# Optimization experiments

Measured on AMD Instinct MI355X. Metric: run time of the kernel, lower is better.

## Reference

```python
import jax, jax.numpy as jnp
import numpy as np

N_USERS = 100000
N_ITEMS = 200000
N_NODES = N_USERS + N_ITEMS
EMB_DIM = 64
N_EDGES = 4000000
N_LAYERS = 2
BATCH = 8192
EMB_REG = 2.5e-5


def setup_inputs() -> dict:
    key = jax.random.key(0)
    k = jax.random.split(key, 7)
    return {
        "user_emb": jax.random.normal(k[0], (N_USERS, EMB_DIM), jnp.float32) * 0.1,
        "item_emb": jax.random.normal(k[1], (N_ITEMS, EMB_DIM), jnp.float32) * 0.1,
        "all_h": jax.random.randint(k[2], (N_EDGES,), 0, N_NODES, jnp.int64 if jax.config.jax_enable_x64 else jnp.int32),
        "all_t": jax.random.randint(k[3], (N_EDGES,), 0, N_NODES, jnp.int64 if jax.config.jax_enable_x64 else jnp.int32),
        "users": jax.random.randint(k[4], (BATCH,), 0, N_USERS),
        "pos_items": jax.random.randint(k[5], (BATCH,), 0, N_ITEMS),
        "neg_items": jax.random.randint(k[6], (BATCH,), 0, N_ITEMS),
    }


def _spmm(h, t, vals, x):
    # out[h] += vals * x[t]  over all edges; [N_NODES, D]
    return jax.ops.segment_sum(vals[:, None] * x[t], h, num_segments=N_NODES)


def reference(user_emb, item_emb, all_h, all_t, users, pos_items, neg_items):
    # symmetric normalization G = D^{-1/2} A D^{-1/2} on the edge list
    deg = jax.ops.segment_sum(jnp.ones((all_h.shape[0],), user_emb.dtype), all_h,
                              num_segments=N_NODES)
    dinv = jnp.where(deg > 0, deg ** -0.5, 0.0)
    g_vals = dinv[all_h] * dinv[all_t]

    # inference1: n_layers of SpMM with residual; sum over all layer outputs
    # (dropout p=0 on the main branch in the source -> identity)
    emb = jnp.concatenate([user_emb, item_emb], axis=0)  # [N, D]
    acc = emb
    for _ in range(N_LAYERS):
        emb = _spmm(all_h, all_t, g_vals, emb) + emb
        acc = acc + emb
    ua, ia = acc[:N_USERS], acc[N_USERS:]

    # BPR loss on the batch
    u = ua[users]
    pos = ia[pos_items]
    neg = ia[neg_items]
    pos_scores = jnp.sum(u * pos, axis=1)
    neg_scores = jnp.sum(u * neg, axis=1)
    mf_loss = jnp.mean(jax.nn.softplus(neg_scores - pos_scores))

    # embedding L2 regularization on the pre-propagation embeddings
    u_pre = user_emb[users]
    pos_pre = item_emb[pos_items]
    neg_pre = item_emb[neg_items]
    emb_loss = EMB_REG * (jnp.sum(u_pre ** 2) + jnp.sum(pos_pre ** 2)
                          + jnp.sum(neg_pre ** 2))
    return (mf_loss, emb_loss)
```

## Files before the change

### kernel.cpp

```cpp
#include <hip/hip_runtime.h>
#include <math.h>

#define N_USERS 100000
#define N_ITEMS 200000
#define N_NODES 300000
#define EMB_DIM 64
#define N_EDGES 4000000
#define BATCH   8192
#define EMB_REG 2.5e-05f

#define BUCK_SH 9
#define BN      512
#define NBUCK   586
#define BSLOT   7424
#define EPB     8192
#define EPT     32
#define NBLK_A  489
#define NBLK_MARK (BATCH / 256)
#define PACK_SH 19
#define SCORE2_BLOCKS (BATCH / 16)

typedef unsigned short u16;
typedef unsigned int   u32;
typedef unsigned char  u8;
typedef __attribute__((ext_vector_type(8))) u16 u16x8;
typedef __attribute__((ext_vector_type(2))) float f32x2;

__device__ __forceinline__ float bf2f(u16 x) {
    u32 u = ((u32)x) << 16;
    return __builtin_bit_cast(float, u);
}
__device__ __forceinline__ u16 f2bf(float f) {
    u32 u = __builtin_bit_cast(u32, f);
    return (u16)((u + 0x7FFFu + ((u >> 16) & 1u)) >> 16);
}

__global__ __launch_bounds__(256) void kA(const int* __restrict__ hh,
                                          const int* __restrict__ tt,
                                          int* __restrict__ bcur, int* __restrict__ gp,
                                          const int* __restrict__ users,
                                          const int* __restrict__ pos,
                                          const int* __restrict__ neg,
                                          u8* __restrict__ flags,
                                          u8* __restrict__ e0s8) {
    if (blockIdx.x >= NBLK_A) {
        int i = (blockIdx.x - NBLK_A) * 256 + threadIdx.x;
        if (i < BATCH) {
            flags[users[i]] = 1;
            flags[N_USERS + pos[i]] = 1;
            flags[N_USERS + neg[i]] = 1;
        }
        if (blockIdx.x == NBLK_A && threadIdx.x < 16)
            ((int*)(e0s8 + (size_t)N_NODES * EMB_DIM))[threadIdx.x] = 0;
        return;
    }
    __shared__ int sh_cnt[NBUCK];
    __shared__ int sh_off[NBUCK];
    __shared__ int sh_base[NBUCK];
    __shared__ int stage[EPB];
    __shared__ u16 sbid[EPB];
    int tid = threadIdx.x;
    for (int j = tid; j < NBUCK; j += 256) sh_cnt[j] = 0;
    __syncthreads();
    int cbase = blockIdx.x * EPB;
    int clen  = min(EPB, N_EDGES - cbase);
    int pk[EPT], bk[EPT];
    #pragma unroll
    for (int j = 0; j < EPT; ++j) {
        int i = j * 256 + tid;
        bk[j] = -1;
        if (i < clen) {
            int h = hh[cbase + i];
            int t = tt[cbase + i];
            int b = h >> BUCK_SH;
            bk[j] = b;
            pk[j] = ((h & (BN - 1)) << PACK_SH) | t;
            atomicAdd(&sh_cnt[b], 1);
        }
    }
    __syncthreads();
    if (tid < 64) {
        int lane = tid, carry = 0;
        for (int b0 = 0; b0 < NBUCK; b0 += 64) {
            int idx = b0 + lane;
            int v = (idx < NBUCK) ? sh_cnt[idx] : 0;
            int incl = v;
            #pragma unroll
            for (int d = 1; d < 64; d <<= 1) {
                int u = __shfl_up(incl, d, 64);
                if (lane >= d) incl += u;
            }
            if (idx < NBUCK) sh_off[idx] = carry + incl - v;
            carry += __shfl(incl, 63, 64);
        }
    }
    __syncthreads();
    for (int j = tid; j < NBUCK; j += 256) {
        int c = sh_cnt[j];
        sh_base[j] = j * BSLOT + (c ? atomicAdd(&bcur[j], c) : 0);
        sh_cnt[j] = 0;
    }
    __syncthreads();
    #pragma unroll
    for (int j = 0; j < EPT; ++j) {
        if (bk[j] >= 0) {
            int r = atomicAdd(&sh_cnt[bk[j]], 1);
            int p = sh_off[bk[j]] + r;
            stage[p] = pk[j];
            sbid[p]  = (u16)bk[j];
        }
    }
    __syncthreads();
    for (int i = tid; i < clen; i += 256) {
        int b = sbid[i];
        gp[sh_base[b] + i - sh_off[b]] = stage[i];
    }
}

__global__ __launch_bounds__(256) void kB(const int* __restrict__ bcur,
                                          int* __restrict__ gp,
                                          int2* __restrict__ sde, float* __restrict__ dinv,
                                          const float* __restrict__ uemb,
                                          const float* __restrict__ iemb,
                                          u8* __restrict__ e0s8) {
    __shared__ int   ncnt[BN];
    __shared__ int   noff[BN];
    __shared__ float sdv[BN];
    __shared__ int   slots[BSLOT];
    int b = blockIdx.x;
    int node0 = b << BUCK_SH;
    int nn = min(BN, N_NODES - node0);
    int base = b * BSLOT;
    int count = bcur[b];
    int tid = threadIdx.x;
    for (int j = tid; j < BN; j += 256) ncnt[j] = 0;
    __syncthreads();
    for (int i = tid; i < count; i += 256)
        atomicAdd(&ncnt[gp[base + i] >> PACK_SH], 1);
    __syncthreads();
    if (tid < 64) {
        int lane = tid, carry = 0;
        #pragma unroll
        for (int b0 = 0; b0 < BN; b0 += 64) {
            int idx = b0 + lane;
            int v = ncnt[idx];
            int incl = v;
            #pragma unroll
            for (int d = 1; d < 64; d <<= 1) {
                int u = __shfl_up(incl, d, 64);
                if (lane >= d) incl += u;
            }
            noff[idx] = carry + incl - v;
            carry += __shfl(incl, 63, 64);
        }
    }
    __syncthreads();
    for (int j = tid; j < nn; j += 256) {
        int c = ncnt[j];
        float dv = c > 0 ? rsqrtf((float)c) : 0.0f;
        sde[node0 + j]  = make_int2(base + noff[j], c);
        dinv[node0 + j] = dv;
        sdv[j] = dv;
    }
    __syncthreads();
    for (int j = tid; j < BN; j += 256) ncnt[j] = noff[j];
    __syncthreads();
    for (int i = tid; i < count; i += 256) {
        int p = gp[base + i];
        int r = atomicAdd(&ncnt[p >> PACK_SH], 1);
        slots[r] = p & ((1 << PACK_SH) - 1);
    }
    __syncthreads();
    for (int i = tid; i < count; i += 256)
        gp[base + i] = slots[i];
    for (int i = tid; i < nn * 8; i += 256) {
        int j = i >> 3;
        float sc = sdv[j];
        int gnode = node0 + j;
        size_t ebase = (size_t)gnode * EMB_DIM + (size_t)(i & 7) * 8;
        const size_t UELEMS = (size_t)N_USERS * EMB_DIM;
        const float* src = (ebase < UELEMS) ? uemb + ebase : iemb + (ebase - UELEMS);
        float4 a  = ((const float4*)src)[0];
        float4 c4 = ((const float4*)src)[1];
        u32 w0 = __builtin_amdgcn_cvt_pk_fp8_f32(sc * a.x,  sc * a.y,  0,  false);
        w0 = __builtin_amdgcn_cvt_pk_fp8_f32(sc * a.z,  sc * a.w,  w0, true);
        u32 w1 = __builtin_amdgcn_cvt_pk_fp8_f32(sc * c4.x, sc * c4.y, 0,  false);
        w1 = __builtin_amdgcn_cvt_pk_fp8_f32(sc * c4.z, sc * c4.w, w1, true);
        uint2 o; o.x = w0; o.y = w1;
        ((uint2*)e0s8)[(size_t)gnode * 8 + (i & 7)] = o;
    }
}

__global__ __launch_bounds__(256) void k_spmm1(const int2* __restrict__ sde,
                        const int* __restrict__ et,
                        const u8* __restrict__ src8,
                        const float* __restrict__ uemb, const float* __restrict__ iemb,
                        const u8* __restrict__ flags,
                        u16* __restrict__ dstb, u8* __restrict__ dst8) {
    int lane = threadIdx.x & 63;
    int g    = lane >> 2;
    int sl   = lane & 3;
    int gb   = lane & 60;
    int node = blockIdx.x * 64 + ((threadIdx.x >> 6) << 4) + g;
    bool alive = node < N_NODES;
    int2 se = alive ? sde[node] : make_int2(0, 0);
    int s = se.x, ne = se.y;
    float dh = ne > 0 ? rsqrtf((float)ne) : 0.0f;
    float acc[16];
    #pragma unroll
    for (int k = 0; k < 16; ++k) acc[k] = 0.f;
    int nb = (ne + 3) & ~3;
    for (int j0 = 0; j0 < nb; j0 += 4) {
        int idx = j0 + sl;
        int ets = (idx < ne) ? et[s + idx] : N_NODES;
        #pragma unroll
        for (int jj = 0; jj < 4; ++jj) {
            int t = __shfl(ets, gb | jj, 64);
            uint4 d8 = ((const uint4*)(src8 + (size_t)t * EMB_DIM))[sl];
            f32x2 p;
            p = __builtin_amdgcn_cvt_pk_f32_fp8(d8.x, false); acc[0]  += p.x; acc[1]  += p.y;
            p = __builtin_amdgcn_cvt_pk_f32_fp8(d8.x, true);  acc[2]  += p.x; acc[3]  += p.y;
            p = __builtin_amdgcn_cvt_pk_f32_fp8(d8.y, false); acc[4]  += p.x; acc[5]  += p.y;
            p = __builtin_amdgcn_cvt_pk_f32_fp8(d8.y, true);  acc[6]  += p.x; acc[7]  += p.y;
            p = __builtin_amdgcn_cvt_pk_f32_fp8(d8.z, false); acc[8]  += p.x; acc[9]  += p.y;
            p = __builtin_amdgcn_cvt_pk_f32_fp8(d8.z, true);  acc[10] += p.x; acc[11] += p.y;
            p = __builtin_amdgcn_cvt_pk_f32_fp8(d8.w, false); acc[12] += p.x; acc[13] += p.y;
            p = __builtin_amdgcn_cvt_pk_f32_fp8(d8.w, true);  acc[14] += p.x; acc[15] += p.y;
        }
    }
    if (!alive) {
        if (node == N_NODES) {
            uint4 z; z.x = 0; z.y = 0; z.z = 0; z.w = 0;
            ((uint4*)(dst8 + (size_t)N_NODES * EMB_DIM))[sl] = z;
        }
        return;
    }
    const float* srow = (node < N_USERS)
        ? uemb + (size_t)node * EMB_DIM
        : iemb + (size_t)(node - N_USERS) * EMB_DIM;
    float4 a0 = ((const float4*)srow)[sl * 4 + 0];
    float4 a1 = ((const float4*)srow)[sl * 4 + 1];
    float4 a2 = ((const float4*)srow)[sl * 4 + 2];
    float4 a3 = ((const float4*)srow)[sl * 4 + 3];
    float v[16];
    v[0]  = dh * acc[0]  + a0.x; v[1]  = dh * acc[1]  + a0.y;
    v[2]  = dh * acc[2]  + a0.z; v[3]  = dh * acc[3]  + a0.w;
    v[4]  = dh * acc[4]  + a1.x; v[5]  = dh * acc[5]  + a1.y;
    v[6]  = dh * acc[6]  + a1.z; v[7]  = dh * acc[7]  + a1.w;
    v[8]  = dh * acc[8]  + a2.x; v[9]  = dh * acc[9]  + a2.y;
    v[10] = dh * acc[10] + a2.z; v[11] = dh * acc[11] + a2.w;
    v[12] = dh * acc[12] + a3.x; v[13] = dh * acc[13] + a3.y;
    v[14] = dh * acc[14] + a3.z; v[15] = dh * acc[15] + a3.w;
    uint4 ow;
    u32 w;
    w = __builtin_amdgcn_cvt_pk_fp8_f32(dh * v[0],  dh * v[1],  0, false);
    w = __builtin_amdgcn_cvt_pk_fp8_f32(dh * v[2],  dh * v[3],  w, true);  ow.x = w;
    w = __builtin_amdgcn_cvt_pk_fp8_f32(dh * v[4],  dh * v[5],  0, false);
    w = __builtin_amdgcn_cvt_pk_fp8_f32(dh * v[6],  dh * v[7],  w, true);  ow.y = w;
    w = __builtin_amdgcn_cvt_pk_fp8_f32(dh * v[8],  dh * v[9],  0, false);
    w = __builtin_amdgcn_cvt_pk_fp8_f32(dh * v[10], dh * v[11], w, true);  ow.z = w;
    w = __builtin_amdgcn_cvt_pk_fp8_f32(dh * v[12], dh * v[13], 0, false);
    w = __builtin_amdgcn_cvt_pk_fp8_f32(dh * v[14], dh * v[15], w, true);  ow.w = w;
    ((uint4*)(dst8 + (size_t)node * EMB_DIM))[sl] = ow;
    if (flags[node]) {
        u16x8 o0, o1;
        o0.s0 = f2bf(v[0]);  o0.s1 = f2bf(v[1]);  o0.s2 = f2bf(v[2]);  o0.s3 = f2bf(v[3]);
        o0.s4 = f2bf(v[4]);  o0.s5 = f2bf(v[5]);  o0.s6 = f2bf(v[6]);  o0.s7 = f2bf(v[7]);
        o1.s0 = f2bf(v[8]);  o1.s1 = f2bf(v[9]);  o1.s2 = f2bf(v[10]); o1.s3 = f2bf(v[11]);
        o1.s4 = f2bf(v[12]); o1.s5 = f2bf(v[13]); o1.s6 = f2bf(v[14]); o1.s7 = f2bf(v[15]);
        ((u16x8*)(dstb + (size_t)node * EMB_DIM))[sl * 2]     = o0;
        ((u16x8*)(dstb + (size_t)node * EMB_DIM))[sl * 2 + 1] = o1;
    }
}

__global__ __launch_bounds__(256) void k_score2(
        const int* __restrict__ users, const int* __restrict__ pos,
        const int* __restrict__ neg,
        const float* __restrict__ uemb, const float* __restrict__ iemb,
        const u16* __restrict__ emb1b, const u8* __restrict__ emb1s8,
        const int2* __restrict__ sde, const int* __restrict__ et,
        const float* __restrict__ dinv,
        float* __restrict__ pmf, float* __restrict__ psq) {
    __shared__ float accL[3 * 16 * 64];
    __shared__ float smf[4], ssq[4];
    int tid  = threadIdx.x;
    int wv   = tid >> 6;
    int lane = tid & 63;
    int g    = lane >> 2;
    int sl   = lane & 3;
    int gb   = lane & 60;
    int B0   = blockIdx.x * 16;

    if (wv < 3) {
        int b = B0 + g;
        int node = (wv == 0) ? users[b]
                 : (wv == 1) ? (N_USERS + pos[b])
                             : (N_USERS + neg[b]);
        int2 se = sde[node];
        int s = se.x, ne = se.y;
        float acc[16];
        #pragma unroll
        for (int i = 0; i < 16; ++i) acc[i] = 0.f;
        int nb = (ne + 3) & ~3;
        for (int j0 = 0; j0 < nb; j0 += 4) {
            int idx = j0 + sl;
            int ets = (idx < ne) ? et[s + idx] : N_NODES;
            #pragma unroll
            for (int jj = 0; jj < 4; ++jj) {
                int t = __shfl(ets, gb | jj, 64);
                uint4 d8 = ((const uint4*)(emb1s8 + (size_t)t * EMB_DIM))[sl];
                f32x2 p;
                p = __builtin_amdgcn_cvt_pk_f32_fp8(d8.x, false); acc[0]  += p.x; acc[1]  += p.y;
                p = __builtin_amdgcn_cvt_pk_f32_fp8(d8.x, true);  acc[2]  += p.x; acc[3]  += p.y;
                p = __builtin_amdgcn_cvt_pk_f32_fp8(d8.y, false); acc[4]  += p.x; acc[5]  += p.y;
                p = __builtin_amdgcn_cvt_pk_f32_fp8(d8.y, true);  acc[6]  += p.x; acc[7]  += p.y;
                p = __builtin_amdgcn_cvt_pk_f32_fp8(d8.z, false); acc[8]  += p.x; acc[9]  += p.y;
                p = __builtin_amdgcn_cvt_pk_f32_fp8(d8.z, true);  acc[10] += p.x; acc[11] += p.y;
                p = __builtin_amdgcn_cvt_pk_f32_fp8(d8.w, false); acc[12] += p.x; acc[13] += p.y;
                p = __builtin_amdgcn_cvt_pk_f32_fp8(d8.w, true);  acc[14] += p.x; acc[15] += p.y;
            }
        }
        float* dst = &accL[((wv * 16 + g) << 6) + (sl << 4)];
        ((float4*)dst)[0] = make_float4(acc[0],  acc[1],  acc[2],  acc[3]);
        ((float4*)dst)[1] = make_float4(acc[4],  acc[5],  acc[6],  acc[7]);
        ((float4*)dst)[2] = make_float4(acc[8],  acc[9],  acc[10], acc[11]);
        ((float4*)dst)[3] = make_float4(acc[12], acc[13], acc[14], acc[15]);
    }
    __syncthreads();
    float mfl = 0.f, sql = 0.f;
    int d = lane;
    #pragma unroll
    for (int q = 0; q < 4; ++q) {
        int bl = wv * 4 + q;
        int b  = B0 + bl;
        int u  = users[b];
        int pi = pos[b];
        int ni = neg[b];
        int n0 = u, n1 = N_USERS + pi, n2 = N_USERS + ni;
        float pre0 = uemb[(size_t)u  * EMB_DIM + d];
        float pre1 = iemb[(size_t)pi * EMB_DIM + d];
        float pre2 = iemb[(size_t)ni * EMB_DIM + d];
        float a0 = pre0 + 2.0f * bf2f(emb1b[(size_t)n0 * EMB_DIM + d])
                 + dinv[n0] * accL[((0 * 16 + bl) << 6) + d];
        float a1 = pre1 + 2.0f * bf2f(emb1b[(size_t)n1 * EMB_DIM + d])
                 + dinv[n1] * accL[((1 * 16 + bl) << 6) + d];
        float a2 = pre2 + 2.0f * bf2f(emb1b[(size_t)n2 * EMB_DIM + d])
                 + dinv[n2] * accL[((2 * 16 + bl) << 6) + d];
        float ps = a0 * a1;
        float ns = a0 * a2;
        float sq = pre0 * pre0 + pre1 * pre1 + pre2 * pre2;
        #pragma unroll
        for (int off2 = 32; off2 > 0; off2 >>= 1) {
            ps += __shfl_down(ps, off2, 64);
            ns += __shfl_down(ns, off2, 64);
            sq += __shfl_down(sq, off2, 64);
        }
        if (lane == 0) {
            float x = ns - ps;
            mfl += fmaxf(x, 0.0f) + log1pf(expf(-fabsf(x)));
            sql += sq;
        }
    }
    if (lane == 0) { smf[wv] = mfl; ssq[wv] = sql; }
    __syncthreads();
    if (tid == 0) {
        pmf[blockIdx.x] = smf[0] + smf[1] + smf[2] + smf[3];
        psq[blockIdx.x] = ssq[0] + ssq[1] + ssq[2] + ssq[3];
    }
}

__global__ void k_final(const float* __restrict__ pmf, const float* __restrict__ psq,
                        float* __restrict__ out) {
    __shared__ float smf[4], ssq[4];
    int tid = threadIdx.x;
    float mf = 0.f, sq = 0.f;
    #pragma unroll
    for (int i = 0; i < SCORE2_BLOCKS / 256; ++i) {
        mf += pmf[tid + i * 256];
        sq += psq[tid + i * 256];
    }
    #pragma unroll
    for (int off2 = 32; off2 > 0; off2 >>= 1) {
        mf += __shfl_down(mf, off2, 64);
        sq += __shfl_down(sq, off2, 64);
    }
    if ((tid & 63) == 0) { smf[tid >> 6] = mf; ssq[tid >> 6] = sq; }
    __syncthreads();
    if (tid == 0) {
        out[0] = (smf[0] + smf[1] + smf[2] + smf[3]) * (1.0f / BATCH);
        out[1] = EMB_REG * (ssq[0] + ssq[1] + ssq[2] + ssq[3]);
    }
}

extern "C" void kernel_launch(void* const* d_in, const int* in_sizes, int n_in,
                              void* d_out, int out_size, void* d_ws, size_t ws_size,
                              hipStream_t stream) {
    const float* uemb  = (const float*)d_in[0];
    const float* iemb  = (const float*)d_in[1];
    const int*   all_h = (const int*)d_in[2];
    const int*   all_t = (const int*)d_in[3];
    const int*   users = (const int*)d_in[4];
    const int*   pos   = (const int*)d_in[5];
    const int*   neg   = (const int*)d_in[6];
    float* out = (float*)d_out;

    int*   ws     = (int*)d_ws;
    float* dinv   = (float*)ws;
    int2*  sde    = (int2*)(ws + 300032);
    u8*    flags  = (u8*)(ws + 900096);
    int*   bcur   = ws + 975104;
    float* pmf    = (float*)(ws + 976128);
    float* psq    = (float*)(ws + 978176);
    int*   gp     = ws + 980224;
    u8*    e0s8   = (u8*)(ws + 5330688);
    u8*    emb1s8 = (u8*)(ws + 10130944);
    u16*   emb1b  = (u16*)(ws + 14930960);

    hipMemsetAsync(flags, 0, 304128, stream);

    kA <<<NBLK_A + NBLK_MARK, 256, 0, stream>>>(all_h, all_t, bcur, gp,
                                                users, pos, neg, flags, e0s8);
    kB <<<NBUCK, 256, 0, stream>>>(bcur, gp, sde, dinv, uemb, iemb, e0s8);

    k_spmm1<<<(N_NODES + 63) / 64, 256, 0, stream>>>(sde, gp, e0s8, uemb, iemb,
                                                     flags, emb1b, emb1s8);

    k_score2<<<SCORE2_BLOCKS, 256, 0, stream>>>(users, pos, neg, uemb, iemb,
                                                emb1b, emb1s8, sde, gp, dinv,
                                                pmf, psq);
    k_final<<<1, 256, 0, stream>>>(pmf, psq, out);
}
```

Measured before the change: 284.3 us.

## Replace two-pass bucketed CSR build with global-atomic histogram, scan, and scatter

The edge list was previously converted to CSR with a two-level bucket sort: block-local shared-memory binning into padded buckets, then per-bucket node sorting in shared memory. This replaces it with a global atomic degree histogram, a two-kernel block-sum scan that also produces dinv and the fp8 scaled embeddings, and a scatter kernel that places each edge tail using an atomic decrement per head node. It removes the padded bucket slots and the shared-memory staging. In exchange it relies on 4M random global atomics, twice over, and adds two extra kernel launches. Edge order within each row becomes nondeterministic.

```diff
diff --git a/kernel.cpp b/kernel.cpp
--- a/kernel.cpp
+++ b/kernel.cpp
@@ -9,15 +9,10 @@
 #define BATCH   8192
 #define EMB_REG 2.5e-05f
 
-#define BUCK_SH 9
-#define BN      512
-#define NBUCK   586
-#define BSLOT   7424
-#define EPB     8192
-#define EPT     32
-#define NBLK_A  489
+#define BN      256
+#define NBUCK   1172
+#define NBLK_H  15625
 #define NBLK_MARK (BATCH / 256)
-#define PACK_SH 19
 #define SCORE2_BLOCKS (BATCH / 16)
 
 typedef unsigned short u16;
@@ -35,144 +30,89 @@
     return (u16)((u + 0x7FFFu + ((u >> 16) & 1u)) >> 16);
 }
 
-__global__ __launch_bounds__(256) void kA(const int* __restrict__ hh,
-                                          const int* __restrict__ tt,
-                                          int* __restrict__ bcur, int* __restrict__ gp,
-                                          const int* __restrict__ users,
-                                          const int* __restrict__ pos,
-                                          const int* __restrict__ neg,
-                                          u8* __restrict__ flags,
-                                          u8* __restrict__ e0s8) {
-    if (blockIdx.x >= NBLK_A) {
-        int i = (blockIdx.x - NBLK_A) * 256 + threadIdx.x;
+__global__ __launch_bounds__(256) void k_hist(const int* __restrict__ hh,
+                                              int* __restrict__ deg,
+                                              const int* __restrict__ users,
+                                              const int* __restrict__ pos,
+                                              const int* __restrict__ neg,
+                                              u8* __restrict__ flags,
+                                              u8* __restrict__ e0s8) {
+    if (blockIdx.x >= NBLK_H) {
+        int i = (blockIdx.x - NBLK_H) * 256 + threadIdx.x;
         if (i < BATCH) {
             flags[users[i]] = 1;
             flags[N_USERS + pos[i]] = 1;
             flags[N_USERS + neg[i]] = 1;
         }
-        if (blockIdx.x == NBLK_A && threadIdx.x < 16)
+        if (blockIdx.x == NBLK_H && threadIdx.x < 16)
             ((int*)(e0s8 + (size_t)N_NODES * EMB_DIM))[threadIdx.x] = 0;
         return;
     }
-    __shared__ int sh_cnt[NBUCK];
-    __shared__ int sh_off[NBUCK];
-    __shared__ int sh_base[NBUCK];
-    __shared__ int stage[EPB];
-    __shared__ u16 sbid[EPB];
+    int i = blockIdx.x * 256 + threadIdx.x;
+    atomicAdd(&deg[hh[i]], 1);
+}
+
+__global__ __launch_bounds__(256) void k_scanA(const int* __restrict__ deg,
+                                               int* __restrict__ bsum) {
+    __shared__ int sw[4];
+    int b = blockIdx.x;
     int tid = threadIdx.x;
-    for (int j = tid; j < NBUCK; j += 256) sh_cnt[j] = 0;
-    __syncthreads();
-    int cbase = blockIdx.x * EPB;
-    int clen  = min(EPB, N_EDGES - cbase);
-    int pk[EPT], bk[EPT];
-    #pragma unroll
-    for (int j = 0; j < EPT; ++j) {
-        int i = j * 256 + tid;
-        bk[j] = -1;
-        if (i < clen) {
-            int h = hh[cbase + i];
-            int t = tt[cbase + i];
-            int b = h >> BUCK_SH;
-            bk[j] = b;
-            pk[j] = ((h & (BN - 1)) << PACK_SH) | t;
-            atomicAdd(&sh_cnt[b], 1);
-        }
-    }
-    __syncthreads();
+    int node = (b << 8) + tid;
+    int v = (node < N_NODES) ? deg[node] : 0;
+    #pragma unroll
+    for (int o = 32; o > 0; o >>= 1) v += __shfl_down(v, o, 64);
+    if ((tid & 63) == 0) sw[tid >> 6] = v;
+    __syncthreads();
+    if (tid == 0) bsum[b] = sw[0] + sw[1] + sw[2] + sw[3];
+}
+
+__global__ __launch_bounds__(256) void k_scanB(const int* __restrict__ deg,
+                                               const int* __restrict__ bsum,
+                                               int2* __restrict__ sde,
+                                               float* __restrict__ dinv,
+                                               const float* __restrict__ uemb,
+                                               const float* __restrict__ iemb,
+                                               u8* __restrict__ e0s8) {
+    __shared__ int   ncnt[BN];
+    __shared__ int   noff[BN];
+    __shared__ float sdv[BN];
+    __shared__ int   sbase[4];
+    int b = blockIdx.x;
+    int node0 = b << 8;
+    int nn = min(BN, N_NODES - node0);
+    int tid = threadIdx.x;
+    int acc = 0;
+    for (int i = tid; i < b; i += 256) acc += bsum[i];
+    #pragma unroll
+    for (int o = 32; o > 0; o >>= 1) acc += __shfl_down(acc, o, 64);
+    if ((tid & 63) == 0) sbase[tid >> 6] = acc;
+    ncnt[tid] = (node0 + tid < N_NODES) ? deg[node0 + tid] : 0;
+    __syncthreads();
+    int base = sbase[0] + sbase[1] + sbase[2] + sbase[3];
     if (tid < 64) {
         int lane = tid, carry = 0;
-        for (int b0 = 0; b0 < NBUCK; b0 += 64) {
-            int idx = b0 + lane;
-            int v = (idx < NBUCK) ? sh_cnt[idx] : 0;
+        #pragma unroll
+        for (int b0 = 0; b0 < BN; b0 += 64) {
+            int v = ncnt[b0 + lane];
             int incl = v;
             #pragma unroll
             for (int d = 1; d < 64; d <<= 1) {
                 int u = __shfl_up(incl, d, 64);
                 if (lane >= d) incl += u;
             }
-            if (idx < NBUCK) sh_off[idx] = carry + incl - v;
+            noff[b0 + lane] = carry + incl - v;
             carry += __shfl(incl, 63, 64);
         }
     }
     __syncthreads();
-    for (int j = tid; j < NBUCK; j += 256) {
-        int c = sh_cnt[j];
-        sh_base[j] = j * BSLOT + (c ? atomicAdd(&bcur[j], c) : 0);
-        sh_cnt[j] = 0;
-    }
-    __syncthreads();
-    #pragma unroll
-    for (int j = 0; j < EPT; ++j) {
-        if (bk[j] >= 0) {
-            int r = atomicAdd(&sh_cnt[bk[j]], 1);
-            int p = sh_off[bk[j]] + r;
-            stage[p] = pk[j];
-            sbid[p]  = (u16)bk[j];
-        }
-    }
-    __syncthreads();
-    for (int i = tid; i < clen; i += 256) {
-        int b = sbid[i];
-        gp[sh_base[b] + i - sh_off[b]] = stage[i];
-    }
-}
-
-__global__ __launch_bounds__(256) void kB(const int* __restrict__ bcur,
-                                          int* __restrict__ gp,
-                                          int2* __restrict__ sde, float* __restrict__ dinv,
-                                          const float* __restrict__ uemb,
-                                          const float* __restrict__ iemb,
-                                          u8* __restrict__ e0s8) {
-    __shared__ int   ncnt[BN];
-    __shared__ int   noff[BN];
-    __shared__ float sdv[BN];
-    __shared__ int   slots[BSLOT];
-    int b = blockIdx.x;
-    int node0 = b << BUCK_SH;
-    int nn = min(BN, N_NODES - node0);
-    int base = b * BSLOT;
-    int count = bcur[b];
-    int tid = threadIdx.x;
-    for (int j = tid; j < BN; j += 256) ncnt[j] = 0;
-    __syncthreads();
-    for (int i = tid; i < count; i += 256)
-        atomicAdd(&ncnt[gp[base + i] >> PACK_SH], 1);
-    __syncthreads();
-    if (tid < 64) {
-        int lane = tid, carry = 0;
-        #pragma unroll
-        for (int b0 = 0; b0 < BN; b0 += 64) {
-            int idx = b0 + lane;
-            int v = ncnt[idx];
-            int incl = v;
-            #pragma unroll
-            for (int d = 1; d < 64; d <<= 1) {
-                int u = __shfl_up(incl, d, 64);
-                if (lane >= d) incl += u;
-            }
-            noff[idx] = carry + incl - v;
-            carry += __shfl(incl, 63, 64);
-        }
-    }
-    __syncthreads();
-    for (int j = tid; j < nn; j += 256) {
-        int c = ncnt[j];
+    if (tid < nn) {
+        int c = ncnt[tid];
         float dv = c > 0 ? rsqrtf((float)c) : 0.0f;
-        sde[node0 + j]  = make_int2(base + noff[j], c);
-        dinv[node0 + j] = dv;
-        sdv[j] = dv;
-    }
-    __syncthreads();
-    for (int j = tid; j < BN; j += 256) ncnt[j] = noff[j];
-    __syncthreads();
-    for (int i = tid; i < count; i += 256) {
-        int p = gp[base + i];
-        int r = atomicAdd(&ncnt[p >> PACK_SH], 1);
-        slots[r] = p & ((1 << PACK_SH) - 1);
-    }
-    __syncthreads();
-    for (int i = tid; i < count; i += 256)
-        gp[base + i] = slots[i];
+        sde[node0 + tid]  = make_int2(base + noff[tid], c);
+        dinv[node0 + tid] = dv;
+        sdv[tid] = dv;
+    }
+    __syncthreads();
     for (int i = tid; i < nn * 8; i += 256) {
         int j = i >> 3;
         float sc = sdv[j];
@@ -189,6 +129,18 @@
         uint2 o; o.x = w0; o.y = w1;
         ((uint2*)e0s8)[(size_t)gnode * 8 + (i & 7)] = o;
     }
+}
+
+__global__ __launch_bounds__(256) void k_scatter(const int* __restrict__ hh,
+                                                 const int* __restrict__ tt,
+                                                 int* __restrict__ deg,
+                                                 const int2* __restrict__ sde,
+                                                 int* __restrict__ et) {
+    int i = blockIdx.x * 256 + threadIdx.x;
+    int h = hh[i];
+    int t = tt[i];
+    int old = atomicSub(&deg[h], 1);
+    et[sde[h].x + old - 1] = t;
 }
 
 __global__ __launch_bounds__(256) void k_spmm1(const int2* __restrict__ sde,
@@ -408,25 +360,29 @@
     float* dinv   = (float*)ws;
     int2*  sde    = (int2*)(ws + 300032);
     u8*    flags  = (u8*)(ws + 900096);
-    int*   bcur   = ws + 975104;
-    float* pmf    = (float*)(ws + 976128);
-    float* psq    = (float*)(ws + 978176);
-    int*   gp     = ws + 980224;
-    u8*    e0s8   = (u8*)(ws + 5330688);
-    u8*    emb1s8 = (u8*)(ws + 10130944);
-    u16*   emb1b  = (u16*)(ws + 14930960);
-
-    hipMemsetAsync(flags, 0, 304128, stream);
-
-    kA <<<NBLK_A + NBLK_MARK, 256, 0, stream>>>(all_h, all_t, bcur, gp,
-                                                users, pos, neg, flags, e0s8);
-    kB <<<NBUCK, 256, 0, stream>>>(bcur, gp, sde, dinv, uemb, iemb, e0s8);
-
-    k_spmm1<<<(N_NODES + 63) / 64, 256, 0, stream>>>(sde, gp, e0s8, uemb, iemb,
+    int*   deg    = ws + 975104;
+    int*   bsum   = ws + 1275136;
+    float* pmf    = (float*)(ws + 1276416);
+    float* psq    = (float*)(ws + 1276928);
+    int*   et     = ws + 1277440;
+    u8*    e0s8   = (u8*)(ws + 5277440);
+    u8*    emb1s8 = (u8*)(ws + 10077456);
+    u16*   emb1b  = (u16*)(ws + 14877472);
+
+    hipMemsetAsync(flags, 0, 1505280, stream);
+
+    k_hist<<<NBLK_H + NBLK_MARK, 256, 0, stream>>>(all_h, deg, users, pos, neg,
+                                                   flags, e0s8);
+    k_scanA<<<NBUCK, 256, 0, stream>>>(deg, bsum);
+    k_scanB<<<NBUCK, 256, 0, stream>>>(deg, bsum, sde, dinv, uemb, iemb, e0s8);
+
+    k_scatter<<<NBLK_H, 256, 0, stream>>>(all_h, all_t, deg, sde, et);
+
+    k_spmm1<<<(N_NODES + 63) / 64, 256, 0, stream>>>(sde, et, e0s8, uemb, iemb,
                                                      flags, emb1b, emb1s8);
 
     k_score2<<<SCORE2_BLOCKS, 256, 0, stream>>>(users, pos, neg, uemb, iemb,
-                                                emb1b, emb1s8, sde, gp, dinv,
+                                                emb1b, emb1s8, sde, et, dinv,
                                                 pmf, psq);
     k_final<<<1, 256, 0, stream>>>(pmf, psq, out);
 }
```

Measured after the change: 587.1 us. 107% more time.
